# Performance work log

Measured on AMD Instinct MI355X. Metric: run time of the kernel, lower is better.

The kernel has to match this reference:

```python
import jax, jax.numpy as jnp
import numpy as np

EMBED_DIM = 1024
NUM_HEAD = 16
HEAD_DIM = EMBED_DIM // NUM_HEAD


def setup_inputs() -> dict:
    key = jax.random.key(0)
    ks = jax.random.split(key, 9)
    B, S, D = 2, 2048, EMBED_DIM
    scale = 1.0 / np.sqrt(D)
    x = jax.random.normal(ks[0], (B, S, D), dtype=jnp.float32)
    Wq = jax.random.normal(ks[1], (D, D), dtype=jnp.float32) * scale
    bq = jnp.zeros((D,), jnp.float32)
    Wk = jax.random.normal(ks[2], (D, D), dtype=jnp.float32) * scale
    bk = jnp.zeros((D,), jnp.float32)
    Wv = jax.random.normal(ks[3], (D, D), dtype=jnp.float32) * scale
    bv = jnp.zeros((D,), jnp.float32)
    Wfc = jax.random.normal(ks[4], (D, D), dtype=jnp.float32) * scale
    bfc = jnp.zeros((D,), jnp.float32)
    return {"x": x, "Wq": Wq, "bq": bq, "Wk": Wk, "bk": bk,
            "Wv": Wv, "bv": bv, "Wfc": Wfc, "bfc": bfc}


def _split_heads(t):
    B, S, D = t.shape
    return t.reshape(B, S, NUM_HEAD, HEAD_DIM).transpose(0, 2, 1, 3)  # b nh s hd


def reference(x, Wq, bq, Wk, bk, Wv, bv, Wfc, bfc):
    # torch nn.Linear: y = x @ W.T + b
    q = _split_heads(x @ Wq.T + bq)   # [b, nh, s, hd]
    k = _split_heads(x @ Wk.T + bk)   # [b, nh, s, hd]
    v = _split_heads(x @ Wv.T + bv)   # [b, nh, s, hd]
    # Gram matrix K^T K per (batch, head): [b, nh, hd, hd]
    gram = jnp.einsum('bnsh,bnsk->bnhk', k, k)
    gram_inv = jnp.linalg.inv(gram)
    # score = Q (K^T K)^{-1} K^T : [b, nh, s, s]
    q_proj = jnp.einsum('bnsh,bnhk->bnsk', q, gram_inv)
    score = jnp.einsum('bnsk,bntk->bnst', q_proj, k)
    attn = jax.nn.softmax(score / jnp.sqrt(jnp.float32(EMBED_DIM)), axis=-1)
    out = jnp.einsum('bnst,bnth->bnsh', attn, v)  # [b, nh, s, hd]
    B, _, S, _ = out.shape
    out = out.transpose(0, 2, 1, 3).reshape(B, S, EMBED_DIM)
    return out @ Wfc.T + bfc
```

## Files before the change

### kernel.cpp

```cpp
#include <hip/hip_runtime.h>
#include <cstddef>
#include <cstdint>

#define S_LEN 2048
#define NHEAD 16
#define HDIM  64
#define EMB   1024
#define MROWS 4096

typedef short bf16x8 __attribute__((ext_vector_type(8)));
typedef float f32x4 __attribute__((ext_vector_type(4)));

__device__ __forceinline__ unsigned short f2bf(float f) {
  union { float f; unsigned u; } v; v.f = f;
  unsigned r = v.u + 0x7FFF + ((v.u >> 16) & 1);
  return (unsigned short)(r >> 16);
}

__device__ __forceinline__ f32x4 fzero() {
  f32x4 z = {0.0f, 0.0f, 0.0f, 0.0f};
  return z;
}

__global__ __launch_bounds__(256) void cast_kernel(
    const float* __restrict__ x, const float* __restrict__ Wq,
    const float* __restrict__ Wk, const float* __restrict__ Wv,
    const float* __restrict__ Wfc, unsigned short* __restrict__ dst)
{
  size_t idx8 = (size_t)(blockIdx.x * 256 + threadIdx.x) * 8;
  unsigned seg = (unsigned)(idx8 >> 20);
  const float* src;
  size_t off;
  if (seg < 4) { src = x; off = idx8; }
  else {
    const float* w4[4] = {Wq, Wk, Wv, Wfc};
    src = w4[seg - 4];
    off = idx8 & 0xFFFFFu;
  }
  float4 a = *(const float4*)&src[off];
  float4 b = *(const float4*)&src[off + 4];
  union { unsigned short h[8]; uint4 u; } p;
  p.h[0] = f2bf(a.x); p.h[1] = f2bf(a.y); p.h[2] = f2bf(a.z); p.h[3] = f2bf(a.w);
  p.h[4] = f2bf(b.x); p.h[5] = f2bf(b.y); p.h[6] = f2bf(b.z); p.h[7] = f2bf(b.w);
  *(uint4*)&dst[idx8] = p.u;
}

__global__ __launch_bounds__(256) void gemm_qkv(
    const unsigned short* __restrict__ A, const unsigned short* __restrict__ Wall,
    const float* __restrict__ bq, const float* __restrict__ bk,
    const float* __restrict__ bv, unsigned short* __restrict__ Qhd,
    unsigned short* __restrict__ Khd, unsigned short* __restrict__ KTd,
    unsigned short* __restrict__ VTd)
{
  __shared__ short As[128][40];
  __shared__ short Bs[128][40];
  const int z = blockIdx.z;
  const unsigned short* B = Wall + (size_t)z * 1048576;
  const float* bias = (z == 0) ? bq : (z == 1) ? bk : bv;
  unsigned short* Yh = (z == 0) ? Qhd : (z == 1) ? Khd : nullptr;
  unsigned short* Yt = (z == 1) ? KTd : (z == 2) ? VTd : nullptr;
  const int K = EMB;
  const int t = threadIdx.x;
  const int lane = t & 63, w = t >> 6;
  const int quad = lane >> 4, l16 = lane & 15;
  const int wr = w >> 1, wc = w & 1;
  const int m0 = blockIdx.y * 128, n0 = blockIdx.x * 128;
  const int sr = t >> 2, sk = (t & 3) * 8;

  f32x4 acc[4][4];
#pragma unroll
  for (int i = 0; i < 4; ++i)
#pragma unroll
    for (int j = 0; j < 4; ++j) acc[i][j] = fzero();

  float4 pa0 = *(const float4*)&A[(size_t)(m0 + sr) * K + sk];
  float4 pa1 = *(const float4*)&A[(size_t)(m0 + 64 + sr) * K + sk];
  float4 pb0 = *(const float4*)&B[(size_t)(n0 + sr) * K + sk];
  float4 pb1 = *(const float4*)&B[(size_t)(n0 + 64 + sr) * K + sk];

  for (int k0 = 0; k0 < K; k0 += 32) {
    __syncthreads();
    *(float4*)&As[sr][sk] = pa0;
    *(float4*)&As[64 + sr][sk] = pa1;
    *(float4*)&Bs[sr][sk] = pb0;
    *(float4*)&Bs[64 + sr][sk] = pb1;
    __syncthreads();
    if (k0 + 32 < K) {
      pa0 = *(const float4*)&A[(size_t)(m0 + sr) * K + k0 + 32 + sk];
      pa1 = *(const float4*)&A[(size_t)(m0 + 64 + sr) * K + k0 + 32 + sk];
      pb0 = *(const float4*)&B[(size_t)(n0 + sr) * K + k0 + 32 + sk];
      pb1 = *(const float4*)&B[(size_t)(n0 + 64 + sr) * K + k0 + 32 + sk];
    }
    bf16x8 af[4], bfr[4];
#pragma unroll
    for (int i = 0; i < 4; ++i)
      af[i] = *(const bf16x8*)&As[64 * wr + 16 * i + l16][quad * 8];
#pragma unroll
    for (int j = 0; j < 4; ++j)
      bfr[j] = *(const bf16x8*)&Bs[64 * wc + 16 * j + l16][quad * 8];
#pragma unroll
    for (int i = 0; i < 4; ++i)
#pragma unroll
      for (int j = 0; j < 4; ++j)
        acc[i][j] = __builtin_amdgcn_mfma_f32_16x16x32_bf16(af[i], bfr[j], acc[i][j], 0, 0, 0);
  }

#pragma unroll
  for (int i = 0; i < 4; ++i) {
    int mb = m0 + 64 * wr + 16 * i + quad * 4;
#pragma unroll
    for (int j = 0; j < 4; ++j) {
      int n = n0 + 64 * wc + 16 * j + l16;
      float bvv = bias[n];
      int h = n >> 6, d = n & 63;
      if (Yh) {
#pragma unroll
        for (int r = 0; r < 4; ++r) {
          int m = mb + r;
          int b = m >> 11, s = m & 2047;
          Yh[((size_t)(b * NHEAD + h)) * 131072 + (size_t)s * 64 + d] =
              f2bf(acc[i][j][r] + bvv);
        }
      }
      if (Yt) {
        int b = mb >> 11, s = mb & 2047;
        unsigned short h0 = f2bf(acc[i][j][0] + bvv);
        unsigned short h1 = f2bf(acc[i][j][1] + bvv);
        unsigned short h2 = f2bf(acc[i][j][2] + bvv);
        unsigned short h3 = f2bf(acc[i][j][3] + bvv);
        uint2 pk;
        pk.x = (unsigned)h0 | ((unsigned)h1 << 16);
        pk.y = (unsigned)h2 | ((unsigned)h3 << 16);
        *(uint2*)&Yt[((size_t)(b * NHEAD + h)) * 131072 + (size_t)d * S_LEN + s] = pk;
      }
    }
  }
}

__global__ __launch_bounds__(256) void gemm_fc(
    const unsigned short* __restrict__ A, const unsigned short* __restrict__ B,
    const float* __restrict__ bias, float* __restrict__ Yf)
{
  __shared__ short As[128][40];
  __shared__ short Bs[128][40];
  const int K = EMB, N = EMB;
  const int t = threadIdx.x;
  const int lane = t & 63, w = t >> 6;
  const int quad = lane >> 4, l16 = lane & 15;
  const int wr = w >> 1, wc = w & 1;
  const int m0 = blockIdx.y * 128, n0 = blockIdx.x * 128;
  const int sr = t >> 2, sk = (t & 3) * 8;

  f32x4 acc[4][4];
#pragma unroll
  for (int i = 0; i < 4; ++i)
#pragma unroll
    for (int j = 0; j < 4; ++j) acc[i][j] = fzero();

  float4 pa0 = *(const float4*)&A[(size_t)(m0 + sr) * K + sk];
  float4 pa1 = *(const float4*)&A[(size_t)(m0 + 64 + sr) * K + sk];
  float4 pb0 = *(const float4*)&B[(size_t)(n0 + sr) * K + sk];
  float4 pb1 = *(const float4*)&B[(size_t)(n0 + 64 + sr) * K + sk];

  for (int k0 = 0; k0 < K; k0 += 32) {
    __syncthreads();
    *(float4*)&As[sr][sk] = pa0;
    *(float4*)&As[64 + sr][sk] = pa1;
    *(float4*)&Bs[sr][sk] = pb0;
    *(float4*)&Bs[64 + sr][sk] = pb1;
    __syncthreads();
    if (k0 + 32 < K) {
      pa0 = *(const float4*)&A[(size_t)(m0 + sr) * K + k0 + 32 + sk];
      pa1 = *(const float4*)&A[(size_t)(m0 + 64 + sr) * K + k0 + 32 + sk];
      pb0 = *(const float4*)&B[(size_t)(n0 + sr) * K + k0 + 32 + sk];
      pb1 = *(const float4*)&B[(size_t)(n0 + 64 + sr) * K + k0 + 32 + sk];
    }
    bf16x8 af[4], bfr[4];
#pragma unroll
    for (int i = 0; i < 4; ++i)
      af[i] = *(const bf16x8*)&As[64 * wr + 16 * i + l16][quad * 8];
#pragma unroll
    for (int j = 0; j < 4; ++j)
      bfr[j] = *(const bf16x8*)&Bs[64 * wc + 16 * j + l16][quad * 8];
#pragma unroll
    for (int i = 0; i < 4; ++i)
#pragma unroll
      for (int j = 0; j < 4; ++j)
        acc[i][j] = __builtin_amdgcn_mfma_f32_16x16x32_bf16(af[i], bfr[j], acc[i][j], 0, 0, 0);
  }

#pragma unroll
  for (int i = 0; i < 4; ++i) {
    int mb = m0 + 64 * wr + 16 * i + quad * 4;
#pragma unroll
    for (int j = 0; j < 4; ++j) {
      int n = n0 + 64 * wc + 16 * j + l16;
      float bvv = bias[n];
#pragma unroll
      for (int r = 0; r < 4; ++r)
        Yf[(size_t)(mb + r) * N + n] = acc[i][j][r] + bvv;
    }
  }
}

__global__ __launch_bounds__(256) void gram_mfma(
    const unsigned short* __restrict__ KTh, float* __restrict__ gram_p)
{
  __shared__ short KTs[64][136];
  const int t = threadIdx.x;
  const int lane = t & 63, w = t >> 6;
  const int quad = lane >> 4, l16 = lane & 15;
  const int bh = blockIdx.x >> 2, part = blockIdx.x & 3;
  const unsigned short* Kb = KTh + (size_t)bh * 131072 + part * 512;

  f32x4 gacc[4];
#pragma unroll
  for (int j = 0; j < 4; ++j) gacc[j] = fzero();

  const int rv = t >> 4, cv = (t & 15) * 8;
  for (int st = 0; st < 4; ++st) {
    float4 vv[4];
#pragma unroll
    for (int r = 0; r < 4; ++r)
      vv[r] = *(const float4*)&Kb[(size_t)(rv + 16 * r) * S_LEN + st * 128 + cv];
    __syncthreads();
#pragma unroll
    for (int r = 0; r < 4; ++r)
      *(float4*)&KTs[rv + 16 * r][cv] = vv[r];
    __syncthreads();
#pragma unroll
    for (int c = 0; c < 4; ++c) {
      bf16x8 ai = *(const bf16x8*)&KTs[16 * w + l16][32 * c + quad * 8];
#pragma unroll
      for (int jb = 0; jb < 4; ++jb) {
        bf16x8 bj = *(const bf16x8*)&KTs[16 * jb + l16][32 * c + quad * 8];
        gacc[jb] = __builtin_amdgcn_mfma_f32_16x16x32_bf16(ai, bj, gacc[jb], 0, 0, 0);
      }
    }
  }
#pragma unroll
  for (int jb = 0; jb < 4; ++jb)
#pragma unroll
    for (int r = 0; r < 4; ++r)
      gram_p[(size_t)blockIdx.x * 4096 +
             (size_t)(16 * w + quad * 4 + r) * 64 + 16 * jb + l16] = gacc[jb][r];
}

__global__ __launch_bounds__(256) void inv_kernel(
    const float* __restrict__ gram_p, unsigned short* __restrict__ ginv)
{
  __shared__ float As[64][68];
  __shared__ float prow[2][64];
  __shared__ float fcol[2][64];
  const int bh = blockIdx.x;
  const int t = threadIdx.x;
  const int r = t >> 2;
  const int c0 = (t & 3) * 16;
  const float* G = gram_p + (size_t)bh * 4 * 4096;

  float4 g[4];
#pragma unroll
  for (int jj = 0; jj < 4; ++jj) {
    int off = r * 64 + c0 + 4 * jj;
    float4 s0 = *(const float4*)&G[off];
    float4 s1 = *(const float4*)&G[4096 + off];
    float4 s2 = *(const float4*)&G[8192 + off];
    float4 s3 = *(const float4*)&G[12288 + off];
    g[jj].x = (s0.x + s1.x) + (s2.x + s3.x);
    g[jj].y = (s0.y + s1.y) + (s2.y + s3.y);
    g[jj].z = (s0.z + s1.z) + (s2.z + s3.z);
    g[jj].w = (s0.w + s1.w) + (s2.w + s3.w);
    *(float4*)&As[r][c0 + 4 * jj] = g[jj];
  }
  if (c0 == 0) fcol[0][r] = g[0].x;
  if (r == 0) {
#pragma unroll
    for (int jj = 0; jj < 4; ++jj) *(float4*)&prow[0][c0 + 4 * jj] = g[jj];
  }
  __syncthreads();

  for (int k = 0; k < 64; ++k) {
    const int kb = k & 1;
    const float f = fcol[kb][r];
    const float ip = 1.0f / fcol[kb][k];
    const float fi = f * ip;
    const bool pr = (r == k);
    float4 nv[4];
#pragma unroll
    for (int jj = 0; jj < 4; ++jj) {
      float4 a = *(const float4*)&As[r][c0 + 4 * jj];
      float4 p = *(const float4*)&prow[kb][c0 + 4 * jj];
      float4 o;
      if (pr) {
        o.x = p.x * ip; o.y = p.y * ip; o.z = p.z * ip; o.w = p.w * ip;
      } else {
        o.x = fmaf(-fi, p.x, a.x); o.y = fmaf(-fi, p.y, a.y);
        o.z = fmaf(-fi, p.z, a.z); o.w = fmaf(-fi, p.w, a.w);
      }
      const int cb = c0 + 4 * jj;
      const float kv = pr ? ip : -fi;
      if (cb == k) o.x = kv;
      if (cb + 1 == k) o.y = kv;
      if (cb + 2 == k) o.z = kv;
      if (cb + 3 == k) o.w = kv;
      *(float4*)&As[r][c0 + 4 * jj] = o;
      nv[jj] = o;
    }
    if (k < 63) {
      const int nk = k + 1, nb = nk & 1;
      if (nk >= c0 && nk < c0 + 16) fcol[nb][r] = As[r][nk];
      if (r == nk) {
#pragma unroll
        for (int jj = 0; jj < 4; ++jj) *(float4*)&prow[nb][c0 + 4 * jj] = nv[jj];
      }
    }
    __syncthreads();
  }

  unsigned short* O = ginv + (size_t)bh * 4096;
#pragma unroll
  for (int jj = 0; jj < 4; ++jj) {
    float4 v = *(const float4*)&As[r][c0 + 4 * jj];
    uint2 pk;
    pk.x = (unsigned)f2bf(v.x) | ((unsigned)f2bf(v.y) << 16);
    pk.y = (unsigned)f2bf(v.z) | ((unsigned)f2bf(v.w) << 16);
    *(uint2*)&O[r * 64 + c0 + 4 * jj] = pk;
  }
}

__global__ __launch_bounds__(256) void flash_mfma(
    const unsigned short* __restrict__ Qh, const unsigned short* __restrict__ Kh,
    const unsigned short* __restrict__ VTh, const unsigned short* __restrict__ Ginv,
    unsigned short* __restrict__ AO)
{
  __shared__ short Ks[128][72];
  __shared__ short VTs[64][136];
  __shared__ short Ps[64][136];
  __shared__ short Qps[64][72];
  __shared__ float Lred[4][64];
  const int t = threadIdx.x;
  const int lane = t & 63, w = t >> 6;
  const int quad = lane >> 4, l16 = lane & 15;
  const int qt = blockIdx.x, bh = blockIdx.y;
  const unsigned short* Qb = Qh + (size_t)bh * 131072;
  const unsigned short* Kb = Kh + (size_t)bh * 131072;
  const unsigned short* Vb = VTh + (size_t)bh * 131072;
  short* G0 = &VTs[0][0];

  {
    int r0 = t >> 3, cq = (t & 7) * 8;
#pragma unroll
    for (int r = 0; r < 2; ++r) {
      int row = r0 + 32 * r;
      *(float4*)&Ks[row][cq] = *(const float4*)&Qb[(size_t)(qt * 64 + row) * 64 + cq];
      *(float4*)&G0[row * 72 + cq] = *(const float4*)&Ginv[(size_t)bh * 4096 + row * 64 + cq];
    }
  }
  __syncthreads();
  {
    f32x4 qacc[4];
#pragma unroll
    for (int nb = 0; nb < 4; ++nb) qacc[nb] = fzero();
#pragma unroll
    for (int c = 0; c < 2; ++c) {
      bf16x8 aq = *(const bf16x8*)&Ks[16 * w + l16][32 * c + quad * 8];
#pragma unroll
      for (int nb = 0; nb < 4; ++nb) {
        bf16x8 bg = *(const bf16x8*)&G0[(16 * nb + l16) * 72 + 32 * c + quad * 8];
        qacc[nb] = __builtin_amdgcn_mfma_f32_16x16x32_bf16(aq, bg, qacc[nb], 0, 0, 0);
      }
    }
    __syncthreads();
#pragma unroll
    for (int nb = 0; nb < 4; ++nb)
#pragma unroll
      for (int r = 0; r < 4; ++r)
        Qps[16 * w + quad * 4 + r][16 * nb + l16] = f2bf(qacc[nb][r]);
  }
  float lsum[4] = {0.0f, 0.0f, 0.0f, 0.0f};
  f32x4 oacc[4];
#pragma unroll
  for (int db = 0; db < 4; ++db) oacc[db] = fzero();
  __syncthreads();

  const float scale = 0.03125f;
  const int rk = t >> 3, ck = (t & 7) * 8;
  const int rv = t >> 4, cv = (t & 15) * 8;

  for (int kt = 0; kt < 16; ++kt) {
    float4 kv[4], vv[4];
#pragma unroll
    for (int r = 0; r < 4; ++r)
      kv[r] = *(const float4*)&Kb[(size_t)(kt * 128 + rk + 32 * r) * 64 + ck];
#pragma unroll
    for (int r = 0; r < 4; ++r)
      vv[r] = *(const float4*)&Vb[(size_t)(rv + 16 * r) * S_LEN + kt * 128 + cv];
#pragma unroll
    for (int r = 0; r < 4; ++r) *(float4*)&Ks[rk + 32 * r][ck] = kv[r];
#pragma unroll
    for (int r = 0; r < 4; ++r) *(float4*)&VTs[rv + 16 * r][cv] = vv[r];
    __syncthreads();

    f32x4 sacc[2][4];
#pragma unroll
    for (int kb = 0; kb < 2; ++kb)
#pragma unroll
      for (int qb = 0; qb < 4; ++qb) sacc[kb][qb] = fzero();
#pragma unroll
    for (int c = 0; c < 2; ++c) {
      bf16x8 ak0 = *(const bf16x8*)&Ks[32 * w + l16][32 * c + quad * 8];
      bf16x8 ak1 = *(const bf16x8*)&Ks[32 * w + 16 + l16][32 * c + quad * 8];
#pragma unroll
      for (int qb = 0; qb < 4; ++qb) {
        bf16x8 bq = *(const bf16x8*)&Qps[16 * qb + l16][32 * c + quad * 8];
        sacc[0][qb] = __builtin_amdgcn_mfma_f32_16x16x32_bf16(ak0, bq, sacc[0][qb], 0, 0, 0);
        sacc[1][qb] = __builtin_amdgcn_mfma_f32_16x16x32_bf16(ak1, bq, sacc[1][qb], 0, 0, 0);
      }
    }
#pragma unroll
    for (int kb = 0; kb < 2; ++kb)
#pragma unroll
      for (int qb = 0; qb < 4; ++qb) {
        float e0 = __expf(sacc[kb][qb][0] * scale);
        float e1 = __expf(sacc[kb][qb][1] * scale);
        float e2 = __expf(sacc[kb][qb][2] * scale);
        float e3 = __expf(sacc[kb][qb][3] * scale);
        lsum[qb] += (e0 + e1) + (e2 + e3);
        uint2 pk;
        pk.x = (unsigned)f2bf(e0) | ((unsigned)f2bf(e1) << 16);
        pk.y = (unsigned)f2bf(e2) | ((unsigned)f2bf(e3) << 16);
        *(uint2*)&Ps[16 * qb + l16][32 * w + 16 * kb + quad * 4] = pk;
      }
    __syncthreads();

#pragma unroll
    for (int c = 0; c < 4; ++c) {
      bf16x8 ap = *(const bf16x8*)&Ps[16 * w + l16][32 * c + quad * 8];
#pragma unroll
      for (int db = 0; db < 4; ++db) {
        bf16x8 bv = *(const bf16x8*)&VTs[16 * db + l16][32 * c + quad * 8];
        oacc[db] = __builtin_amdgcn_mfma_f32_16x16x32_bf16(ap, bv, oacc[db], 0, 0, 0);
      }
    }
    __syncthreads();
  }

#pragma unroll
  for (int qb = 0; qb < 4; ++qb) {
    lsum[qb] += __shfl_xor(lsum[qb], 16, 64);
    lsum[qb] += __shfl_xor(lsum[qb], 32, 64);
  }
  if (lane < 16)
#pragma unroll
    for (int qb = 0; qb < 4; ++qb) Lred[w][qb * 16 + l16] = lsum[qb];
  __syncthreads();
  if (t < 64)
    Lred[0][t] = 1.0f / (Lred[0][t] + Lred[1][t] + Lred[2][t] + Lred[3][t]);
  __syncthreads();

  const int b = bh >> 4, h = bh & 15;
#pragma unroll
  for (int r = 0; r < 4; ++r) {
    int q = 16 * w + quad * 4 + r;
    float li = Lred[0][q];
    int s = qt * 64 + q;
    size_t base = (size_t)b * S_LEN * EMB + (size_t)s * EMB + h * 64;
#pragma unroll
    for (int db = 0; db < 4; ++db)
      AO[base + 16 * db + l16] = f2bf(oacc[db][r] * li);
  }
}

extern "C" void kernel_launch(void* const* d_in, const int* in_sizes, int n_in,
                              void* d_out, int out_size, void* d_ws, size_t ws_size,
                              hipStream_t stream) {
  (void)in_sizes; (void)n_in; (void)out_size; (void)ws_size;
  const float* x   = (const float*)d_in[0];
  const float* Wq  = (const float*)d_in[1];
  const float* bq  = (const float*)d_in[2];
  const float* Wk  = (const float*)d_in[3];
  const float* bk  = (const float*)d_in[4];
  const float* Wv  = (const float*)d_in[5];
  const float* bv  = (const float*)d_in[6];
  const float* Wfc = (const float*)d_in[7];
  const float* bfc = (const float*)d_in[8];
  float* out = (float*)d_out;

  unsigned short* xb   = (unsigned short*)d_ws;
  unsigned short* Wqb  = xb + (size_t)4194304;
  unsigned short* Wfcb = Wqb + 3 * 1048576;
  unsigned short* Qhd  = Wfcb + 1048576;
  unsigned short* Khd  = Qhd + 4194304;
  unsigned short* KTd  = Khd + 4194304;
  unsigned short* VTd  = KTd + 4194304;
  unsigned short* AOd  = VTd + 4194304;
  float* gram_p        = (float*)(AOd + 4194304);
  unsigned short* ginv = (unsigned short*)(gram_p + 524288);

  cast_kernel<<<4096, 256, 0, stream>>>(x, Wq, Wk, Wv, Wfc, xb);
  gemm_qkv<<<dim3(8, 32, 3), 256, 0, stream>>>(xb, Wqb, bq, bk, bv,
                                               Qhd, Khd, KTd, VTd);
  gram_mfma<<<128, 256, 0, stream>>>(KTd, gram_p);
  inv_kernel<<<32, 256, 0, stream>>>(gram_p, ginv);
  flash_mfma<<<dim3(S_LEN / 64, 32), 256, 0, stream>>>(Qhd, Khd, VTd, ginv, AOd);
  gemm_fc<<<dim3(8, 32), 256, 0, stream>>>(AOd, Wfcb, bfc, out);
}
```

Baseline: 298.7 us.

## Swizzle flash LDS, prefetch next K/V tile, compute row sums via MFMA

```diff
diff --git a/kernel.cpp b/kernel.cpp
--- a/kernel.cpp
+++ b/kernel.cpp
@@ -13,13 +13,23 @@
 
 __device__ __forceinline__ unsigned short f2bf(float f) {
   union { float f; unsigned u; } v; v.f = f;
-  unsigned r = v.u + 0x7FFF + ((v.u >> 16) & 1);
-  return (unsigned short)(r >> 16);
+  return (unsigned short)((v.u + 0x8000u) >> 16);
+}
+__device__ __forceinline__ unsigned pack2bf(float a, float b) {
+  union { float f; unsigned u; } x, y; x.f = a; y.f = b;
+  return ((x.u + 0x8000u) >> 16) | ((y.u + 0x8000u) & 0xFFFF0000u);
 }
 
 __device__ __forceinline__ f32x4 fzero() {
   f32x4 z = {0.0f, 0.0f, 0.0f, 0.0f};
   return z;
+}
+
+__device__ __forceinline__ int sw64(int row, int col) {
+  return row * 64 + ((((col >> 3) ^ row) & 7) << 3) + (col & 7);
+}
+__device__ __forceinline__ int sw128(int row, int col) {
+  return row * 128 + ((((col >> 3) ^ row) & 15) << 3) + (col & 7);
 }
 
 __global__ __launch_bounds__(256) void cast_kernel(
@@ -39,10 +49,12 @@
   }
   float4 a = *(const float4*)&src[off];
   float4 b = *(const float4*)&src[off + 4];
-  union { unsigned short h[8]; uint4 u; } p;
-  p.h[0] = f2bf(a.x); p.h[1] = f2bf(a.y); p.h[2] = f2bf(a.z); p.h[3] = f2bf(a.w);
-  p.h[4] = f2bf(b.x); p.h[5] = f2bf(b.y); p.h[6] = f2bf(b.z); p.h[7] = f2bf(b.w);
-  *(uint4*)&dst[idx8] = p.u;
+  uint4 p;
+  p.x = pack2bf(a.x, a.y);
+  p.y = pack2bf(a.z, a.w);
+  p.z = pack2bf(b.x, b.y);
+  p.w = pack2bf(b.z, b.w);
+  *(uint4*)&dst[idx8] = p;
 }
 
 __global__ __launch_bounds__(256) void gemm_qkv(
@@ -124,13 +136,9 @@
       }
       if (Yt) {
         int b = mb >> 11, s = mb & 2047;
-        unsigned short h0 = f2bf(acc[i][j][0] + bvv);
-        unsigned short h1 = f2bf(acc[i][j][1] + bvv);
-        unsigned short h2 = f2bf(acc[i][j][2] + bvv);
-        unsigned short h3 = f2bf(acc[i][j][3] + bvv);
         uint2 pk;
-        pk.x = (unsigned)h0 | ((unsigned)h1 << 16);
-        pk.y = (unsigned)h2 | ((unsigned)h3 << 16);
+        pk.x = pack2bf(acc[i][j][0] + bvv, acc[i][j][1] + bvv);
+        pk.y = pack2bf(acc[i][j][2] + bvv, acc[i][j][3] + bvv);
         *(uint2*)&Yt[((size_t)(b * NHEAD + h)) * 131072 + (size_t)d * S_LEN + s] = pk;
       }
     }
@@ -322,8 +330,8 @@
   for (int jj = 0; jj < 4; ++jj) {
     float4 v = *(const float4*)&As[r][c0 + 4 * jj];
     uint2 pk;
-    pk.x = (unsigned)f2bf(v.x) | ((unsigned)f2bf(v.y) << 16);
-    pk.y = (unsigned)f2bf(v.z) | ((unsigned)f2bf(v.w) << 16);
+    pk.x = pack2bf(v.x, v.y);
+    pk.y = pack2bf(v.z, v.w);
     *(uint2*)&O[r * 64 + c0 + 4 * jj] = pk;
   }
 }
@@ -333,11 +341,10 @@
     const unsigned short* __restrict__ VTh, const unsigned short* __restrict__ Ginv,
     unsigned short* __restrict__ AO)
 {
-  __shared__ short Ks[128][72];
-  __shared__ short VTs[64][136];
-  __shared__ short Ps[64][136];
-  __shared__ short Qps[64][72];
-  __shared__ float Lred[4][64];
+  __shared__ __align__(16) short Ks[128 * 64];
+  __shared__ __align__(16) short VTs[64 * 128];
+  __shared__ __align__(16) short Ps[64 * 128];
+  __shared__ __align__(16) short Qps[64 * 64];
   const int t = threadIdx.x;
   const int lane = t & 63, w = t >> 6;
   const int quad = lane >> 4, l16 = lane & 15;
@@ -345,61 +352,79 @@
   const unsigned short* Qb = Qh + (size_t)bh * 131072;
   const unsigned short* Kb = Kh + (size_t)bh * 131072;
   const unsigned short* Vb = VTh + (size_t)bh * 131072;
-  short* G0 = &VTs[0][0];
+
+  const int rk = t >> 3, ck = (t & 7) * 8;
+  const int rv = t >> 4, cv = (t & 15) * 8;
+  float4 kv[4], vv[4];
 
   {
     int r0 = t >> 3, cq = (t & 7) * 8;
+    float4 qv[2], gv[2];
 #pragma unroll
     for (int r = 0; r < 2; ++r) {
       int row = r0 + 32 * r;
-      *(float4*)&Ks[row][cq] = *(const float4*)&Qb[(size_t)(qt * 64 + row) * 64 + cq];
-      *(float4*)&G0[row * 72 + cq] = *(const float4*)&Ginv[(size_t)bh * 4096 + row * 64 + cq];
+      qv[r] = *(const float4*)&Qb[(size_t)(qt * 64 + row) * 64 + cq];
+      gv[r] = *(const float4*)&Ginv[(size_t)bh * 4096 + row * 64 + cq];
+    }
+#pragma unroll
+    for (int r = 0; r < 4; ++r)
+      kv[r] = *(const float4*)&Kb[(size_t)(rk + 32 * r) * 64 + ck];
+#pragma unroll
+    for (int r = 0; r < 4; ++r)
+      vv[r] = *(const float4*)&Vb[(size_t)(rv + 16 * r) * S_LEN + cv];
+#pragma unroll
+    for (int r = 0; r < 2; ++r) {
+      int row = r0 + 32 * r;
+      *(float4*)&Ks[sw64(row, cq)] = qv[r];
+      *(float4*)&VTs[sw128(row, cq)] = gv[r];
     }
   }
   __syncthreads();
+
   {
     f32x4 qacc[4];
 #pragma unroll
     for (int nb = 0; nb < 4; ++nb) qacc[nb] = fzero();
 #pragma unroll
     for (int c = 0; c < 2; ++c) {
-      bf16x8 aq = *(const bf16x8*)&Ks[16 * w + l16][32 * c + quad * 8];
+      bf16x8 aq = *(const bf16x8*)&Ks[sw64(16 * w + l16, 32 * c + quad * 8)];
 #pragma unroll
       for (int nb = 0; nb < 4; ++nb) {
-        bf16x8 bg = *(const bf16x8*)&G0[(16 * nb + l16) * 72 + 32 * c + quad * 8];
+        bf16x8 bg = *(const bf16x8*)&VTs[sw128(16 * nb + l16, 32 * c + quad * 8)];
         qacc[nb] = __builtin_amdgcn_mfma_f32_16x16x32_bf16(aq, bg, qacc[nb], 0, 0, 0);
       }
     }
-    __syncthreads();
 #pragma unroll
     for (int nb = 0; nb < 4; ++nb)
 #pragma unroll
+      for (int r = 0; r < 4; ++r) {
+        int row = 16 * w + quad * 4 + r;
+        int col = 16 * nb + l16;
+        Qps[sw64(row, col)] = (short)f2bf(qacc[nb][r]);
+      }
+  }
+  f32x4 oacc[4];
+#pragma unroll
+  for (int db = 0; db < 4; ++db) oacc[db] = fzero();
+  f32x4 lacc = fzero();
+  const bf16x8 ones = {16256, 16256, 16256, 16256, 16256, 16256, 16256, 16256};
+  const float scale = 0.03125f;
+  __syncthreads();
+
+  for (int kt = 0; kt < 16; ++kt) {
+#pragma unroll
+    for (int r = 0; r < 4; ++r) *(float4*)&Ks[sw64(rk + 32 * r, ck)] = kv[r];
+#pragma unroll
+    for (int r = 0; r < 4; ++r) *(float4*)&VTs[sw128(rv + 16 * r, cv)] = vv[r];
+    __syncthreads();
+    if (kt < 15) {
+#pragma unroll
       for (int r = 0; r < 4; ++r)
-        Qps[16 * w + quad * 4 + r][16 * nb + l16] = f2bf(qacc[nb][r]);
-  }
-  float lsum[4] = {0.0f, 0.0f, 0.0f, 0.0f};
-  f32x4 oacc[4];
-#pragma unroll
-  for (int db = 0; db < 4; ++db) oacc[db] = fzero();
-  __syncthreads();
-
-  const float scale = 0.03125f;
-  const int rk = t >> 3, ck = (t & 7) * 8;
-  const int rv = t >> 4, cv = (t & 15) * 8;
-
-  for (int kt = 0; kt < 16; ++kt) {
-    float4 kv[4], vv[4];
-#pragma unroll
-    for (int r = 0; r < 4; ++r)
-      kv[r] = *(const float4*)&Kb[(size_t)(kt * 128 + rk + 32 * r) * 64 + ck];
-#pragma unroll
-    for (int r = 0; r < 4; ++r)
-      vv[r] = *(const float4*)&Vb[(size_t)(rv + 16 * r) * S_LEN + kt * 128 + cv];
-#pragma unroll
-    for (int r = 0; r < 4; ++r) *(float4*)&Ks[rk + 32 * r][ck] = kv[r];
-#pragma unroll
-    for (int r = 0; r < 4; ++r) *(float4*)&VTs[rv + 16 * r][cv] = vv[r];
-    __syncthreads();
+        kv[r] = *(const float4*)&Kb[(size_t)((kt + 1) * 128 + rk + 32 * r) * 64 + ck];
+#pragma unroll
+      for (int r = 0; r < 4; ++r)
+        vv[r] = *(const float4*)&Vb[(size_t)(rv + 16 * r) * S_LEN + (kt + 1) * 128 + cv];
+    }
 
     f32x4 sacc[2][4];
 #pragma unroll
@@ -408,11 +433,11 @@
       for (int qb = 0; qb < 4; ++qb) sacc[kb][qb] = fzero();
 #pragma unroll
     for (int c = 0; c < 2; ++c) {
-      bf16x8 ak0 = *(const bf16x8*)&Ks[32 * w + l16][32 * c + quad * 8];
-      bf16x8 ak1 = *(const bf16x8*)&Ks[32 * w + 16 + l16][32 * c + quad * 8];
+      bf16x8 ak0 = *(const bf16x8*)&Ks[sw64(32 * w + l16, 32 * c + quad * 8)];
+      bf16x8 ak1 = *(const bf16x8*)&Ks[sw64(32 * w + 16 + l16, 32 * c + quad * 8)];
 #pragma unroll
       for (int qb = 0; qb < 4; ++qb) {
-        bf16x8 bq = *(const bf16x8*)&Qps[16 * qb + l16][32 * c + quad * 8];
+        bf16x8 bq = *(const bf16x8*)&Qps[sw64(16 * qb + l16, 32 * c + quad * 8)];
         sacc[0][qb] = __builtin_amdgcn_mfma_f32_16x16x32_bf16(ak0, bq, sacc[0][qb], 0, 0, 0);
         sacc[1][qb] = __builtin_amdgcn_mfma_f32_16x16x32_bf16(ak1, bq, sacc[1][qb], 0, 0, 0);
       }
@@ -425,44 +450,33 @@
         float e1 = __expf(sacc[kb][qb][1] * scale);
         float e2 = __expf(sacc[kb][qb][2] * scale);
         float e3 = __expf(sacc[kb][qb][3] * scale);
-        lsum[qb] += (e0 + e1) + (e2 + e3);
         uint2 pk;
-        pk.x = (unsigned)f2bf(e0) | ((unsigned)f2bf(e1) << 16);
-        pk.y = (unsigned)f2bf(e2) | ((unsigned)f2bf(e3) << 16);
-        *(uint2*)&Ps[16 * qb + l16][32 * w + 16 * kb + quad * 4] = pk;
+        pk.x = pack2bf(e0, e1);
+        pk.y = pack2bf(e2, e3);
+        int row = 16 * qb + l16;
+        int col = 32 * w + 16 * kb + 4 * quad;
+        *(uint2*)&Ps[sw128(row, col)] = pk;
       }
     __syncthreads();
 
 #pragma unroll
     for (int c = 0; c < 4; ++c) {
-      bf16x8 ap = *(const bf16x8*)&Ps[16 * w + l16][32 * c + quad * 8];
+      bf16x8 ap = *(const bf16x8*)&Ps[sw128(16 * w + l16, 32 * c + quad * 8)];
+      lacc = __builtin_amdgcn_mfma_f32_16x16x32_bf16(ap, ones, lacc, 0, 0, 0);
 #pragma unroll
       for (int db = 0; db < 4; ++db) {
-        bf16x8 bv = *(const bf16x8*)&VTs[16 * db + l16][32 * c + quad * 8];
+        bf16x8 bv = *(const bf16x8*)&VTs[sw128(16 * db + l16, 32 * c + quad * 8)];
         oacc[db] = __builtin_amdgcn_mfma_f32_16x16x32_bf16(ap, bv, oacc[db], 0, 0, 0);
       }
     }
     __syncthreads();
   }
 
-#pragma unroll
-  for (int qb = 0; qb < 4; ++qb) {
-    lsum[qb] += __shfl_xor(lsum[qb], 16, 64);
-    lsum[qb] += __shfl_xor(lsum[qb], 32, 64);
-  }
-  if (lane < 16)
-#pragma unroll
-    for (int qb = 0; qb < 4; ++qb) Lred[w][qb * 16 + l16] = lsum[qb];
-  __syncthreads();
-  if (t < 64)
-    Lred[0][t] = 1.0f / (Lred[0][t] + Lred[1][t] + Lred[2][t] + Lred[3][t]);
-  __syncthreads();
-
   const int b = bh >> 4, h = bh & 15;
 #pragma unroll
   for (int r = 0; r < 4; ++r) {
+    float li = 1.0f / lacc[r];
     int q = 16 * w + quad * 4 + r;
-    float li = Lred[0][q];
     int s = qt * 64 + q;
     size_t base = (size_t)b * S_LEN * EMB + (size_t)s * EMB + h * 64;
 #pragma unroll
```

Result: slower. 337.6 us (+13.0%).

## Restructure flash kernel to load K/V straight into registers with double-buffered P

Applied to the files above, without the earlier changes.

```diff
diff --git a/kernel.cpp b/kernel.cpp
--- a/kernel.cpp
+++ b/kernel.cpp
@@ -13,8 +13,11 @@
 
 __device__ __forceinline__ unsigned short f2bf(float f) {
   union { float f; unsigned u; } v; v.f = f;
-  unsigned r = v.u + 0x7FFF + ((v.u >> 16) & 1);
-  return (unsigned short)(r >> 16);
+  return (unsigned short)((v.u + 0x8000u) >> 16);
+}
+__device__ __forceinline__ unsigned pack2bf(float a, float b) {
+  union { float f; unsigned u; } x, y; x.f = a; y.f = b;
+  return ((x.u + 0x8000u) >> 16) | ((y.u + 0x8000u) & 0xFFFF0000u);
 }
 
 __device__ __forceinline__ f32x4 fzero() {
@@ -39,10 +42,12 @@
   }
   float4 a = *(const float4*)&src[off];
   float4 b = *(const float4*)&src[off + 4];
-  union { unsigned short h[8]; uint4 u; } p;
-  p.h[0] = f2bf(a.x); p.h[1] = f2bf(a.y); p.h[2] = f2bf(a.z); p.h[3] = f2bf(a.w);
-  p.h[4] = f2bf(b.x); p.h[5] = f2bf(b.y); p.h[6] = f2bf(b.z); p.h[7] = f2bf(b.w);
-  *(uint4*)&dst[idx8] = p.u;
+  uint4 p;
+  p.x = pack2bf(a.x, a.y);
+  p.y = pack2bf(a.z, a.w);
+  p.z = pack2bf(b.x, b.y);
+  p.w = pack2bf(b.z, b.w);
+  *(uint4*)&dst[idx8] = p;
 }
 
 __global__ __launch_bounds__(256) void gemm_qkv(
@@ -124,13 +129,9 @@
       }
       if (Yt) {
         int b = mb >> 11, s = mb & 2047;
-        unsigned short h0 = f2bf(acc[i][j][0] + bvv);
-        unsigned short h1 = f2bf(acc[i][j][1] + bvv);
-        unsigned short h2 = f2bf(acc[i][j][2] + bvv);
-        unsigned short h3 = f2bf(acc[i][j][3] + bvv);
         uint2 pk;
-        pk.x = (unsigned)h0 | ((unsigned)h1 << 16);
-        pk.y = (unsigned)h2 | ((unsigned)h3 << 16);
+        pk.x = pack2bf(acc[i][j][0] + bvv, acc[i][j][1] + bvv);
+        pk.y = pack2bf(acc[i][j][2] + bvv, acc[i][j][3] + bvv);
         *(uint2*)&Yt[((size_t)(b * NHEAD + h)) * 131072 + (size_t)d * S_LEN + s] = pk;
       }
     }
@@ -322,8 +323,8 @@
   for (int jj = 0; jj < 4; ++jj) {
     float4 v = *(const float4*)&As[r][c0 + 4 * jj];
     uint2 pk;
-    pk.x = (unsigned)f2bf(v.x) | ((unsigned)f2bf(v.y) << 16);
-    pk.y = (unsigned)f2bf(v.z) | ((unsigned)f2bf(v.w) << 16);
+    pk.x = pack2bf(v.x, v.y);
+    pk.y = pack2bf(v.z, v.w);
     *(uint2*)&O[r * 64 + c0 + 4 * jj] = pk;
   }
 }
@@ -333,10 +334,8 @@
     const unsigned short* __restrict__ VTh, const unsigned short* __restrict__ Ginv,
     unsigned short* __restrict__ AO)
 {
-  __shared__ short Ks[128][72];
-  __shared__ short VTs[64][136];
-  __shared__ short Ps[64][136];
-  __shared__ short Qps[64][72];
+  __shared__ short Qps[64 * 72];
+  __shared__ short Ps[2][64 * 72];
   __shared__ float Lred[4][64];
   const int t = threadIdx.x;
   const int lane = t & 63, w = t >> 6;
@@ -345,104 +344,81 @@
   const unsigned short* Qb = Qh + (size_t)bh * 131072;
   const unsigned short* Kb = Kh + (size_t)bh * 131072;
   const unsigned short* Vb = VTh + (size_t)bh * 131072;
-  short* G0 = &VTs[0][0];
+  const unsigned short* Gb = Ginv + (size_t)bh * 4096;
 
   {
-    int r0 = t >> 3, cq = (t & 7) * 8;
-#pragma unroll
-    for (int r = 0; r < 2; ++r) {
-      int row = r0 + 32 * r;
-      *(float4*)&Ks[row][cq] = *(const float4*)&Qb[(size_t)(qt * 64 + row) * 64 + cq];
-      *(float4*)&G0[row * 72 + cq] = *(const float4*)&Ginv[(size_t)bh * 4096 + row * 64 + cq];
-    }
+    bf16x8 aq[2];
+#pragma unroll
+    for (int c = 0; c < 2; ++c)
+      aq[c] = *(const bf16x8*)&Qb[(size_t)(qt * 64 + 16 * w + l16) * 64 + 32 * c + 8 * quad];
+    f32x4 qacc[4];
+#pragma unroll
+    for (int nb = 0; nb < 4; ++nb) qacc[nb] = fzero();
+#pragma unroll
+    for (int c = 0; c < 2; ++c) {
+#pragma unroll
+      for (int nb = 0; nb < 4; ++nb) {
+        bf16x8 bg = *(const bf16x8*)&Gb[(size_t)(16 * nb + l16) * 64 + 32 * c + 8 * quad];
+        qacc[nb] = __builtin_amdgcn_mfma_f32_16x16x32_bf16(aq[c], bg, qacc[nb], 0, 0, 0);
+      }
+    }
+#pragma unroll
+    for (int nb = 0; nb < 4; ++nb)
+#pragma unroll
+      for (int r = 0; r < 4; ++r)
+        Qps[(16 * w + 4 * quad + r) * 72 + 16 * nb + l16] =
+            (short)f2bf(qacc[nb][r] * 0.03125f);
   }
   __syncthreads();
-  {
-    f32x4 qacc[4];
-#pragma unroll
-    for (int nb = 0; nb < 4; ++nb) qacc[nb] = fzero();
+
+  f32x4 oacc[4];
+#pragma unroll
+  for (int qb = 0; qb < 4; ++qb) oacc[qb] = fzero();
+  float lsum[4] = {0.0f, 0.0f, 0.0f, 0.0f};
+
+  for (int kt = 0; kt < 32; ++kt) {
+    bf16x8 ak[2];
+#pragma unroll
+    for (int c = 0; c < 2; ++c)
+      ak[c] = *(const bf16x8*)&Kb[(size_t)(kt * 64 + 16 * w + l16) * 64 + 32 * c + 8 * quad];
+    f32x4 sacc[4];
+#pragma unroll
+    for (int qb = 0; qb < 4; ++qb) sacc[qb] = fzero();
 #pragma unroll
     for (int c = 0; c < 2; ++c) {
-      bf16x8 aq = *(const bf16x8*)&Ks[16 * w + l16][32 * c + quad * 8];
-#pragma unroll
-      for (int nb = 0; nb < 4; ++nb) {
-        bf16x8 bg = *(const bf16x8*)&G0[(16 * nb + l16) * 72 + 32 * c + quad * 8];
-        qacc[nb] = __builtin_amdgcn_mfma_f32_16x16x32_bf16(aq, bg, qacc[nb], 0, 0, 0);
-      }
-    }
-    __syncthreads();
-#pragma unroll
-    for (int nb = 0; nb < 4; ++nb)
-#pragma unroll
-      for (int r = 0; r < 4; ++r)
-        Qps[16 * w + quad * 4 + r][16 * nb + l16] = f2bf(qacc[nb][r]);
-  }
-  float lsum[4] = {0.0f, 0.0f, 0.0f, 0.0f};
-  f32x4 oacc[4];
-#pragma unroll
-  for (int db = 0; db < 4; ++db) oacc[db] = fzero();
-  __syncthreads();
-
-  const float scale = 0.03125f;
-  const int rk = t >> 3, ck = (t & 7) * 8;
-  const int rv = t >> 4, cv = (t & 15) * 8;
-
-  for (int kt = 0; kt < 16; ++kt) {
-    float4 kv[4], vv[4];
-#pragma unroll
-    for (int r = 0; r < 4; ++r)
-      kv[r] = *(const float4*)&Kb[(size_t)(kt * 128 + rk + 32 * r) * 64 + ck];
-#pragma unroll
-    for (int r = 0; r < 4; ++r)
-      vv[r] = *(const float4*)&Vb[(size_t)(rv + 16 * r) * S_LEN + kt * 128 + cv];
-#pragma unroll
-    for (int r = 0; r < 4; ++r) *(float4*)&Ks[rk + 32 * r][ck] = kv[r];
-#pragma unroll
-    for (int r = 0; r < 4; ++r) *(float4*)&VTs[rv + 16 * r][cv] = vv[r];
-    __syncthreads();
-
-    f32x4 sacc[2][4];
-#pragma unroll
-    for (int kb = 0; kb < 2; ++kb)
-#pragma unroll
-      for (int qb = 0; qb < 4; ++qb) sacc[kb][qb] = fzero();
+#pragma unroll
+      for (int qb = 0; qb < 4; ++qb) {
+        bf16x8 bq = *(const bf16x8*)&Qps[(16 * qb + l16) * 72 + 32 * c + 8 * quad];
+        sacc[qb] = __builtin_amdgcn_mfma_f32_16x16x32_bf16(ak[c], bq, sacc[qb], 0, 0, 0);
+      }
+    }
+    short* Pbuf = &Ps[kt & 1][0];
+#pragma unroll
+    for (int qb = 0; qb < 4; ++qb) {
+      float e0 = __expf(sacc[qb][0]);
+      float e1 = __expf(sacc[qb][1]);
+      float e2 = __expf(sacc[qb][2]);
+      float e3 = __expf(sacc[qb][3]);
+      lsum[qb] += (e0 + e1) + (e2 + e3);
+      uint2 pk;
+      pk.x = pack2bf(e0, e1);
+      pk.y = pack2bf(e2, e3);
+      *(uint2*)&Pbuf[(16 * qb + l16) * 72 + 16 * w + 4 * quad] = pk;
+    }
+    __syncthreads();
+
+    bf16x8 av[2];
+#pragma unroll
+    for (int c = 0; c < 2; ++c)
+      av[c] = *(const bf16x8*)&Vb[(size_t)(16 * w + l16) * S_LEN + kt * 64 + 32 * c + 8 * quad];
 #pragma unroll
     for (int c = 0; c < 2; ++c) {
-      bf16x8 ak0 = *(const bf16x8*)&Ks[32 * w + l16][32 * c + quad * 8];
-      bf16x8 ak1 = *(const bf16x8*)&Ks[32 * w + 16 + l16][32 * c + quad * 8];
 #pragma unroll
       for (int qb = 0; qb < 4; ++qb) {
-        bf16x8 bq = *(const bf16x8*)&Qps[16 * qb + l16][32 * c + quad * 8];
-        sacc[0][qb] = __builtin_amdgcn_mfma_f32_16x16x32_bf16(ak0, bq, sacc[0][qb], 0, 0, 0);
-        sacc[1][qb] = __builtin_amdgcn_mfma_f32_16x16x32_bf16(ak1, bq, sacc[1][qb], 0, 0, 0);
-      }
-    }
-#pragma unroll
-    for (int kb = 0; kb < 2; ++kb)
-#pragma unroll
-      for (int qb = 0; qb < 4; ++qb) {
-        float e0 = __expf(sacc[kb][qb][0] * scale);
-        float e1 = __expf(sacc[kb][qb][1] * scale);
-        float e2 = __expf(sacc[kb][qb][2] * scale);
-        float e3 = __expf(sacc[kb][qb][3] * scale);
-        lsum[qb] += (e0 + e1) + (e2 + e3);
-        uint2 pk;
-        pk.x = (unsigned)f2bf(e0) | ((unsigned)f2bf(e1) << 16);
-        pk.y = (unsigned)f2bf(e2) | ((unsigned)f2bf(e3) << 16);
-        *(uint2*)&Ps[16 * qb + l16][32 * w + 16 * kb + quad * 4] = pk;
-      }
-    __syncthreads();
-
-#pragma unroll
-    for (int c = 0; c < 4; ++c) {
-      bf16x8 ap = *(const bf16x8*)&Ps[16 * w + l16][32 * c + quad * 8];
-#pragma unroll
-      for (int db = 0; db < 4; ++db) {
-        bf16x8 bv = *(const bf16x8*)&VTs[16 * db + l16][32 * c + quad * 8];
-        oacc[db] = __builtin_amdgcn_mfma_f32_16x16x32_bf16(ap, bv, oacc[db], 0, 0, 0);
-      }
-    }
-    __syncthreads();
+        bf16x8 bp = *(const bf16x8*)&Pbuf[(16 * qb + l16) * 72 + 32 * c + 8 * quad];
+        oacc[qb] = __builtin_amdgcn_mfma_f32_16x16x32_bf16(av[c], bp, oacc[qb], 0, 0, 0);
+      }
+    }
   }
 
 #pragma unroll
@@ -460,14 +436,13 @@
 
   const int b = bh >> 4, h = bh & 15;
 #pragma unroll
-  for (int r = 0; r < 4; ++r) {
-    int q = 16 * w + quad * 4 + r;
-    float li = Lred[0][q];
-    int s = qt * 64 + q;
-    size_t base = (size_t)b * S_LEN * EMB + (size_t)s * EMB + h * 64;
-#pragma unroll
-    for (int db = 0; db < 4; ++db)
-      AO[base + 16 * db + l16] = f2bf(oacc[db][r] * li);
+  for (int qb = 0; qb < 4; ++qb) {
+    float li = Lred[0][16 * qb + l16];
+    int s = qt * 64 + 16 * qb + l16;
+    size_t base = (size_t)b * S_LEN * EMB + (size_t)s * EMB + h * 64 + 16 * w + 4 * quad;
+#pragma unroll
+    for (int r = 0; r < 4; ++r)
+      AO[base + r] = f2bf(oacc[qb][r] * li);
   }
 }
 
```

After: 285.9 us. 4.3% less time.
